# Kernel tuning notes

Hardware: AMD Instinct MI355X
Metric: run time of the kernel (lower is better)

## Reference

```python
import jax, jax.numpy as jnp
import numpy as np

N_NODES = 100000
N_EDGES = 400000
D = 128           # vector_dim
N_GRAPHS = 4096
N_LAYERS = 5
IN_FEAT = 11


def setup_inputs() -> dict:
    key = jax.random.key(0)
    ks = jax.random.split(key, 6)
    x = jax.random.uniform(ks[0], (N_NODES, IN_FEAT), dtype=jnp.float32)
    edge_index = jax.random.randint(ks[1], (2, N_EDGES), 0, N_NODES, dtype=jnp.int64)
    batch = jnp.sort(jax.random.randint(ks[2], (N_NODES,), 0, N_GRAPHS, dtype=jnp.int64))
    # expansion Linear(11, D)
    We = jax.random.normal(ks[3], (IN_FEAT, D), dtype=jnp.float32) * (1.0 / np.sqrt(IN_FEAT))
    be = jnp.zeros((D,), dtype=jnp.float32)
    # stacked GCNConv weights/biases for 5 layers
    Wg = jax.random.normal(ks[4], (N_LAYERS, D, D), dtype=jnp.float32) * (1.0 / np.sqrt(D))
    bg = jnp.zeros((N_LAYERS, D), dtype=jnp.float32)
    return {"x": x, "edge_index": edge_index, "batch": batch, "num_graphs": N_GRAPHS,
            "We": We, "be": be, "Wg": Wg, "bg": bg}


def reference(x, edge_index, batch, num_graphs, We, be, Wg, bg):
    n = x.shape[0]
    src, dst = edge_index[0], edge_index[1]
    # GCNConv(improved=True): self-loop weight 2 -> deg[i] = in_degree + 2
    deg = jax.ops.segment_sum(jnp.ones((src.shape[0],), x.dtype), dst, num_segments=n) + 2.0
    dinv = deg ** -0.5
    enorm = dinv[src] * dinv[dst]          # per-edge symmetric norm [E]
    self_norm = 2.0 * dinv * dinv          # self-loop contribution [N]

    h = jnp.log(x + 1.0) @ We + be         # expansion [N, D]
    for l in range(Wg.shape[0]):
        t = h @ Wg[l]                      # [N, D]
        agg = jax.ops.segment_sum(t[src] * enorm[:, None], dst, num_segments=n)
        agg = agg + self_norm[:, None] * t + bg[l]
        h = h + jax.nn.relu(agg)           # residual; dropout = identity (eval)
    return jax.ops.segment_sum(h, batch, num_segments=num_graphs)  # global_add_pool [G, D]
```

## Files before the change

### kernel.cpp

```cpp
#include <hip/hip_runtime.h>
#include <hip/hip_bf16.h>

#define NN 100000
#define NE 400000
#define DD 128
#define NG 4096
#define NL 5
#define NF 11
#define GROWS 100096

typedef __attribute__((ext_vector_type(8))) __bf16 bf16x8;
typedef __attribute__((ext_vector_type(4))) float f32x4;


__global__ void deg_kernel(const int* __restrict__ ei, int* __restrict__ deg) {
    int e = blockIdx.x * 256 + threadIdx.x;
    if (e < NE) atomicAdd(&deg[ei[NE + e]], 1);
}

__global__ void scan1_kernel(const int* __restrict__ deg, int* __restrict__ off,
                             int* __restrict__ bsums) {
    __shared__ int lds[256];
    int tid = threadIdx.x, b = blockIdx.x;
    int base = b * 1024 + tid * 4;
    int v[4];
#pragma unroll
    for (int q = 0; q < 4; ++q) {
        int i = base + q;
        v[q] = (i < NN) ? deg[i] : 0;
    }
    int s = v[0] + v[1] + v[2] + v[3];
    lds[tid] = s;
    __syncthreads();
    for (int o = 1; o < 256; o <<= 1) {
        int t2 = (tid >= o) ? lds[tid - o] : 0;
        __syncthreads();
        lds[tid] += t2;
        __syncthreads();
    }
    int p = lds[tid] - s;
#pragma unroll
    for (int q = 0; q < 4; ++q) {
        int i = base + q;
        if (i < NN) off[i] = p;
        p += v[q];
    }
    if (tid == 255) bsums[b] = lds[255];
}

__global__ void scan2_kernel(int* __restrict__ bsums, int nb) {
    __shared__ int lds[128];
    int tid = threadIdx.x;
    int v = (tid < nb) ? bsums[tid] : 0;
    lds[tid] = v;
    __syncthreads();
    for (int o = 1; o < 128; o <<= 1) {
        int t2 = (tid >= o) ? lds[tid - o] : 0;
        __syncthreads();
        lds[tid] += t2;
        __syncthreads();
    }
    if (tid < nb) bsums[tid] = lds[tid] - v;
}

__global__ void finish_kernel(int* __restrict__ off, const int* __restrict__ bsums,
                              const int* __restrict__ deg, float* __restrict__ dinv) {
    int i = blockIdx.x * 256 + threadIdx.x;
    if (i == 0) off[NN] = NE;
    if (i < NN) {
        off[i] += bsums[i >> 10];
        dinv[i] = rsqrtf((float)deg[i] + 2.0f);
    }
}

__global__ void fill_kernel(const int* __restrict__ ei, const int* __restrict__ off,
                            int* __restrict__ cursor, int2* __restrict__ csr,
                            const float* __restrict__ dinv) {
    int e = blockIdx.x * 256 + threadIdx.x;
    if (e >= NE) return;
    int s = ei[e];
    int d = ei[NE + e];
    int pos = off[d] + atomicAdd(&cursor[d], 1);
    csr[pos] = make_int2(s, __float_as_int(dinv[s] * dinv[d]));
}


__global__ void wpack_kernel(const float* __restrict__ Wg, unsigned short* __restrict__ whi,
                             unsigned short* __restrict__ wlo) {
    int t = blockIdx.x * 256 + threadIdx.x;
    int l = t >> 14, r = t & 16383;
    int k = r >> 7, n = r & 127;
    float w = Wg[(size_t)l * 16384 + k * 128 + n];
    __bf16 hb = (__bf16)w;
    float lo = w - (float)hb;
    __bf16 lb = (__bf16)lo;
    int ft = n >> 4, kc = k >> 5, lane = (((k >> 3) & 3) << 4) | (n & 15), i = k & 7;
    size_t idx = (size_t)l * 16384 + (((ft * 4 + kc) * 64 + lane) * 8 + i);
    whi[idx] = __builtin_bit_cast(unsigned short, hb);
    wlo[idx] = __builtin_bit_cast(unsigned short, lb);
}


__global__ __launch_bounds__(256) void expand_kernel(const float* __restrict__ x,
                                                     const float* __restrict__ We,
                                                     const float* __restrict__ be,
                                                     float* __restrict__ h) {
    __shared__ float ls[2 * NF];
    const int tid = threadIdx.x;
    const int node0 = blockIdx.x * 2;
    if (tid < 2 * NF) ls[tid] = __logf(x[(size_t)node0 * NF + tid] + 1.0f);
    __syncthreads();
    const int row = tid >> 7, j = tid & 127;
    float acc = be[j];
#pragma unroll
    for (int f = 0; f < NF; ++f) {
        acc = fmaf(ls[row * NF + f], We[f * DD + j], acc);
    }
    h[(size_t)(node0 + row) * DD + j] = acc;
}


__global__ __launch_bounds__(256) void agg_kernel(const float* __restrict__ h,
                                                  unsigned short* __restrict__ gbh,
                                                  unsigned short* __restrict__ gbl,
                                                  const int* __restrict__ off,
                                                  const int2* __restrict__ csr,
                                                  const float* __restrict__ dinv) {
    const int tid = threadIdx.x;
    const int node = blockIdx.x * 8 + (tid >> 5);
    const int jj = tid & 31;
    const float4* __restrict__ h4 = (const float4*)h;

    float di = dinv[node];
    float sn = 2.0f * di * di;
    float4 hv = h4[(size_t)node * 32 + jj];
    float4 acc = make_float4(sn * hv.x, sn * hv.y, sn * hv.z, sn * hv.w);

    const int e0 = off[node];
    const int e1 = off[node + 1];
#pragma unroll 1
    for (int e = e0; e < e1; e += 4) {
        const int eL = e1 - 1;
        int2 r0 = csr[e];
        int2 r1 = csr[min(e + 1, eL)];
        int2 r2 = csr[min(e + 2, eL)];
        int2 r3 = csr[min(e + 3, eL)];
        float4 v0 = h4[(size_t)r0.x * 32 + jj];
        float4 v1 = h4[(size_t)r1.x * 32 + jj];
        float4 v2 = h4[(size_t)r2.x * 32 + jj];
        float4 v3 = h4[(size_t)r3.x * 32 + jj];
        float w0 = __int_as_float(r0.y);
        float w1 = (e + 1 < e1) ? __int_as_float(r1.y) : 0.f;
        float w2 = (e + 2 < e1) ? __int_as_float(r2.y) : 0.f;
        float w3 = (e + 3 < e1) ? __int_as_float(r3.y) : 0.f;
        acc.x = fmaf(w0, v0.x, acc.x); acc.y = fmaf(w0, v0.y, acc.y);
        acc.z = fmaf(w0, v0.z, acc.z); acc.w = fmaf(w0, v0.w, acc.w);
        acc.x = fmaf(w1, v1.x, acc.x); acc.y = fmaf(w1, v1.y, acc.y);
        acc.z = fmaf(w1, v1.z, acc.z); acc.w = fmaf(w1, v1.w, acc.w);
        acc.x = fmaf(w2, v2.x, acc.x); acc.y = fmaf(w2, v2.y, acc.y);
        acc.z = fmaf(w2, v2.z, acc.z); acc.w = fmaf(w2, v2.w, acc.w);
        acc.x = fmaf(w3, v3.x, acc.x); acc.y = fmaf(w3, v3.y, acc.y);
        acc.z = fmaf(w3, v3.z, acc.z); acc.w = fmaf(w3, v3.w, acc.w);
    }

    __bf16 h0 = (__bf16)acc.x; __bf16 l0 = (__bf16)(acc.x - (float)h0);
    __bf16 h1 = (__bf16)acc.y; __bf16 l1 = (__bf16)(acc.y - (float)h1);
    __bf16 h2 = (__bf16)acc.z; __bf16 l2 = (__bf16)(acc.z - (float)h2);
    __bf16 h3 = (__bf16)acc.w; __bf16 l3 = (__bf16)(acc.w - (float)h3);
    const int tile = node >> 4;
    const int kc = jj >> 3;
    const int kg = (jj >> 1) & 3;
    const int i0 = (jj & 1) * 4;
    const int lanep = (kg << 4) | (node & 15);
    size_t base = (((size_t)tile * 4 + kc) * 64 + lanep) * 8 + i0;
    ushort4 hs = make_ushort4(__builtin_bit_cast(unsigned short, h0),
                              __builtin_bit_cast(unsigned short, h1),
                              __builtin_bit_cast(unsigned short, h2),
                              __builtin_bit_cast(unsigned short, h3));
    ushort4 ls = make_ushort4(__builtin_bit_cast(unsigned short, l0),
                              __builtin_bit_cast(unsigned short, l1),
                              __builtin_bit_cast(unsigned short, l2),
                              __builtin_bit_cast(unsigned short, l3));
    *(ushort4*)(gbh + base) = hs;
    *(ushort4*)(gbl + base) = ls;
}


__global__ __launch_bounds__(256) void mfma_gemm(const unsigned short* __restrict__ gbh,
                                                 const unsigned short* __restrict__ gbl,
                                                 float* __restrict__ h,
                                                 const unsigned short* __restrict__ whi,
                                                 const unsigned short* __restrict__ wlo,
                                                 const float* __restrict__ b) {
    const int lane = threadIdx.x & 63;
    const int wv = threadIdx.x >> 6;
    const int nbase = blockIdx.x * 64 + wv * 16;
    const size_t tbase = ((size_t)(nbase >> 4) * 4 * 64 + lane) * 8;

    bf16x8 gh[4], gl[4];
#pragma unroll
    for (int kc = 0; kc < 4; ++kc) {
        gh[kc] = *(const bf16x8*)(gbh + tbase + kc * 512);
        gl[kc] = *(const bf16x8*)(gbl + tbase + kc * 512);
    }

    f32x4 c[8];
#pragma unroll
    for (int ft = 0; ft < 8; ++ft) c[ft] = (f32x4){0.f, 0.f, 0.f, 0.f};

#pragma unroll
    for (int kc = 0; kc < 4; ++kc) {
#pragma unroll
        for (int ft = 0; ft < 8; ++ft) {
            size_t boff = (size_t)(((ft * 4 + kc) * 64 + lane) * 8);
            bf16x8 wh = *(const bf16x8*)(whi + boff);
            bf16x8 wl = *(const bf16x8*)(wlo + boff);
            c[ft] = __builtin_amdgcn_mfma_f32_16x16x32_bf16(wh, gh[kc], c[ft], 0, 0, 0);
            c[ft] = __builtin_amdgcn_mfma_f32_16x16x32_bf16(wl, gh[kc], c[ft], 0, 0, 0);
            c[ft] = __builtin_amdgcn_mfma_f32_16x16x32_bf16(wh, gl[kc], c[ft], 0, 0, 0);
        }
    }

    const int node = nbase + (lane & 15);
    const int f0 = (lane >> 4) * 4;
    if (node < NN) {
#pragma unroll
        for (int ft = 0; ft < 8; ++ft) {
            size_t o = (size_t)node * DD + ft * 16 + f0;
            float4 hv = *(const float4*)(h + o);
            float4 bv = *(const float4*)(b + ft * 16 + f0);
            hv.x += fmaxf(c[ft][0] + bv.x, 0.f);
            hv.y += fmaxf(c[ft][1] + bv.y, 0.f);
            hv.z += fmaxf(c[ft][2] + bv.z, 0.f);
            hv.w += fmaxf(c[ft][3] + bv.w, 0.f);
            *(float4*)(h + o) = hv;
        }
    }
}


__global__ void pool_kernel(const float* __restrict__ h, const int* __restrict__ batch,
                            float* __restrict__ out) {
    int j = threadIdx.x;
    int n0 = blockIdx.x * 64;
    float acc = 0.f;
    int prev = -1;
    for (int n = 0; n < 64; ++n) {
        int i = n0 + n;
        if (i >= NN) break;
        int bi = batch[i];
        if (bi != prev) {
            if (prev >= 0) atomicAdd(&out[(size_t)prev * DD + j], acc);
            acc = 0.f;
            prev = bi;
        }
        acc += h[(size_t)i * DD + j];
    }
    if (prev >= 0) atomicAdd(&out[(size_t)prev * DD + j], acc);
}


static inline size_t align_up(size_t x, size_t a) { return (x + a - 1) & ~(a - 1); }

extern "C" void kernel_launch(void* const* d_in, const int* in_sizes, int n_in,
                              void* d_out, int out_size, void* d_ws, size_t ws_size,
                              hipStream_t stream) {
    const float* x   = (const float*)d_in[0];
    const int*   ei  = (const int*)d_in[1];
    const int*   bat = (const int*)d_in[2];
    const float* We  = (const float*)d_in[4];
    const float* be  = (const float*)d_in[5];
    const float* Wg  = (const float*)d_in[6];
    const float* bg  = (const float*)d_in[7];
    float* out = (float*)d_out;

    char* p = (char*)d_ws;
    size_t o = 0;
    float* h = (float*)(p + o);       o = align_up(o + (size_t)NN * DD * 4, 512);
    unsigned short* gbh = (unsigned short*)(p + o); o = align_up(o + (size_t)GROWS * DD * 2, 512);
    unsigned short* gbl = (unsigned short*)(p + o); o = align_up(o + (size_t)GROWS * DD * 2, 512);
    float* dinv = (float*)(p + o);    o = align_up(o + (size_t)NN * 4, 512);
    int* deg = (int*)(p + o);         o = align_up(o + (size_t)NN * 4, 512);
    int* cursor = (int*)(p + o);      o = align_up(o + (size_t)NN * 4, 512);
    int* off = (int*)(p + o);         o = align_up(o + (size_t)(NN + 1) * 4, 512);
    int* bsums = (int*)(p + o);       o = align_up(o + 512, 512);
    int2* csr = (int2*)(p + o);       o = align_up(o + (size_t)NE * 8, 512);
    unsigned short* whi = (unsigned short*)(p + o); o = align_up(o + (size_t)NL * 16384 * 2, 512);
    unsigned short* wlo = (unsigned short*)(p + o); o = align_up(o + (size_t)NL * 16384 * 2, 512);
    (void)ws_size; (void)in_sizes; (void)n_in; (void)out_size;

    const int GRID_E = (NE + 255) / 256;
    const int GRID_SCAN1 = (NN + 1023) / 1024;
    const int GRID_N256 = (NN + 255) / 256;
    const int GRID_EXP = NN / 2;
    const int GRID_AGG = NN / 8;
    const int GRID_GEMM = GROWS / 64;
    const int GRID_POOL = (NN + 63) / 64;
    const int GRID_WPACK = NL * 16384 / 256;

    hipMemsetAsync(deg, 0, (size_t)NN * 4, stream);
    hipMemsetAsync(cursor, 0, (size_t)NN * 4, stream);
    hipMemsetAsync(out, 0, (size_t)NG * DD * 4, stream);

    deg_kernel<<<GRID_E, 256, 0, stream>>>(ei, deg);
    scan1_kernel<<<GRID_SCAN1, 256, 0, stream>>>(deg, off, bsums);
    scan2_kernel<<<1, 128, 0, stream>>>(bsums, GRID_SCAN1);
    finish_kernel<<<GRID_N256, 256, 0, stream>>>(off, bsums, deg, dinv);
    fill_kernel<<<GRID_E, 256, 0, stream>>>(ei, off, cursor, csr, dinv);
    wpack_kernel<<<GRID_WPACK, 256, 0, stream>>>(Wg, whi, wlo);

    expand_kernel<<<GRID_EXP, 256, 0, stream>>>(x, We, be, h);

    for (int l = 0; l < NL; ++l) {
        agg_kernel<<<GRID_AGG, 256, 0, stream>>>(h, gbh, gbl, off, csr, dinv);
        mfma_gemm<<<GRID_GEMM, 256, 0, stream>>>(gbh, gbl, h,
                                                 whi + (size_t)l * 16384,
                                                 wlo + (size_t)l * 16384,
                                                 bg + (size_t)l * DD);
    }

    pool_kernel<<<GRID_POOL, 128, 0, stream>>>(h, bat, out);
}
```

Baseline: 601.9 us.

## Drop cursor array via in-place offset atomics, batch expand and widen GEMM tiles

The CSR fill now atomically bumps the exclusive offsets in place, so afterwards off[d] holds the end of segment d. The aggregation reads the segment as off[node-1]..off[node], which removes the cursor buffer and its memset. The expansion kernel handles 8 nodes per block and keeps the We column in registers to reuse it. The MFMA GEMM handles 32 nodes per wave instead of 16, reusing each loaded weight fragment across two node tiles at the cost of more registers.

```diff
diff --git a/kernel.cpp b/kernel.cpp
--- a/kernel.cpp
+++ b/kernel.cpp
@@ -66,21 +66,19 @@
 __global__ void finish_kernel(int* __restrict__ off, const int* __restrict__ bsums,
                               const int* __restrict__ deg, float* __restrict__ dinv) {
     int i = blockIdx.x * 256 + threadIdx.x;
-    if (i == 0) off[NN] = NE;
     if (i < NN) {
         off[i] += bsums[i >> 10];
         dinv[i] = rsqrtf((float)deg[i] + 2.0f);
     }
 }
 
-__global__ void fill_kernel(const int* __restrict__ ei, const int* __restrict__ off,
-                            int* __restrict__ cursor, int2* __restrict__ csr,
-                            const float* __restrict__ dinv) {
+__global__ void fill_kernel(const int* __restrict__ ei, int* __restrict__ off,
+                            int2* __restrict__ csr, const float* __restrict__ dinv) {
     int e = blockIdx.x * 256 + threadIdx.x;
     if (e >= NE) return;
     int s = ei[e];
     int d = ei[NE + e];
-    int pos = off[d] + atomicAdd(&cursor[d], 1);
+    int pos = atomicAdd(&off[d], 1);
     csr[pos] = make_int2(s, __float_as_int(dinv[s] * dinv[d]));
 }
 
@@ -105,18 +103,23 @@
                                                      const float* __restrict__ We,
                                                      const float* __restrict__ be,
                                                      float* __restrict__ h) {
-    __shared__ float ls[2 * NF];
+    __shared__ float ls[8 * NF];
     const int tid = threadIdx.x;
-    const int node0 = blockIdx.x * 2;
-    if (tid < 2 * NF) ls[tid] = __logf(x[(size_t)node0 * NF + tid] + 1.0f);
+    const int node0 = blockIdx.x * 8;
+    if (tid < 8 * NF) ls[tid] = __logf(x[(size_t)node0 * NF + tid] + 1.0f);
     __syncthreads();
-    const int row = tid >> 7, j = tid & 127;
-    float acc = be[j];
-#pragma unroll
-    for (int f = 0; f < NF; ++f) {
-        acc = fmaf(ls[row * NF + f], We[f * DD + j], acc);
-    }
-    h[(size_t)(node0 + row) * DD + j] = acc;
+    const int j = tid & 127;
+    float wv[NF], acc0 = be[j];
+#pragma unroll
+    for (int f = 0; f < NF; ++f) wv[f] = We[f * DD + j];
+#pragma unroll
+    for (int r = 0; r < 4; ++r) {
+        const int nl = r * 2 + (tid >> 7);
+        float acc = acc0;
+#pragma unroll
+        for (int f = 0; f < NF; ++f) acc = fmaf(ls[nl * NF + f], wv[f], acc);
+        h[(size_t)(node0 + nl) * DD + j] = acc;
+    }
 }
 
 
@@ -136,8 +139,8 @@
     float4 hv = h4[(size_t)node * 32 + jj];
     float4 acc = make_float4(sn * hv.x, sn * hv.y, sn * hv.z, sn * hv.w);
 
-    const int e0 = off[node];
-    const int e1 = off[node + 1];
+    const int e0 = (node == 0) ? 0 : off[node - 1];
+    const int e1 = off[node];
 #pragma unroll 1
     for (int e = e0; e < e1; e += 4) {
         const int eL = e1 - 1;
@@ -173,16 +176,14 @@
     const int i0 = (jj & 1) * 4;
     const int lanep = (kg << 4) | (node & 15);
     size_t base = (((size_t)tile * 4 + kc) * 64 + lanep) * 8 + i0;
-    ushort4 hs = make_ushort4(__builtin_bit_cast(unsigned short, h0),
-                              __builtin_bit_cast(unsigned short, h1),
-                              __builtin_bit_cast(unsigned short, h2),
-                              __builtin_bit_cast(unsigned short, h3));
-    ushort4 ls = make_ushort4(__builtin_bit_cast(unsigned short, l0),
-                              __builtin_bit_cast(unsigned short, l1),
-                              __builtin_bit_cast(unsigned short, l2),
-                              __builtin_bit_cast(unsigned short, l3));
-    *(ushort4*)(gbh + base) = hs;
-    *(ushort4*)(gbl + base) = ls;
+    *(ushort4*)(gbh + base) = make_ushort4(__builtin_bit_cast(unsigned short, h0),
+                                           __builtin_bit_cast(unsigned short, h1),
+                                           __builtin_bit_cast(unsigned short, h2),
+                                           __builtin_bit_cast(unsigned short, h3));
+    *(ushort4*)(gbl + base) = make_ushort4(__builtin_bit_cast(unsigned short, l0),
+                                           __builtin_bit_cast(unsigned short, l1),
+                                           __builtin_bit_cast(unsigned short, l2),
+                                           __builtin_bit_cast(unsigned short, l3));
 }
 
 
@@ -194,19 +195,23 @@
                                                  const float* __restrict__ b) {
     const int lane = threadIdx.x & 63;
     const int wv = threadIdx.x >> 6;
-    const int nbase = blockIdx.x * 64 + wv * 16;
+    const int nbase = blockIdx.x * 128 + wv * 32;
     const size_t tbase = ((size_t)(nbase >> 4) * 4 * 64 + lane) * 8;
 
-    bf16x8 gh[4], gl[4];
-#pragma unroll
-    for (int kc = 0; kc < 4; ++kc) {
-        gh[kc] = *(const bf16x8*)(gbh + tbase + kc * 512);
-        gl[kc] = *(const bf16x8*)(gbl + tbase + kc * 512);
-    }
-
-    f32x4 c[8];
-#pragma unroll
-    for (int ft = 0; ft < 8; ++ft) c[ft] = (f32x4){0.f, 0.f, 0.f, 0.f};
+    bf16x8 gh[2][4], gl[2][4];
+#pragma unroll
+    for (int nt = 0; nt < 2; ++nt)
+#pragma unroll
+        for (int kc = 0; kc < 4; ++kc) {
+            gh[nt][kc] = *(const bf16x8*)(gbh + tbase + nt * 2048 + kc * 512);
+            gl[nt][kc] = *(const bf16x8*)(gbl + tbase + nt * 2048 + kc * 512);
+        }
+
+    f32x4 c[2][8];
+#pragma unroll
+    for (int nt = 0; nt < 2; ++nt)
+#pragma unroll
+        for (int ft = 0; ft < 8; ++ft) c[nt][ft] = (f32x4){0.f, 0.f, 0.f, 0.f};
 
 #pragma unroll
     for (int kc = 0; kc < 4; ++kc) {
@@ -215,25 +220,31 @@
             size_t boff = (size_t)(((ft * 4 + kc) * 64 + lane) * 8);
             bf16x8 wh = *(const bf16x8*)(whi + boff);
             bf16x8 wl = *(const bf16x8*)(wlo + boff);
-            c[ft] = __builtin_amdgcn_mfma_f32_16x16x32_bf16(wh, gh[kc], c[ft], 0, 0, 0);
-            c[ft] = __builtin_amdgcn_mfma_f32_16x16x32_bf16(wl, gh[kc], c[ft], 0, 0, 0);
-            c[ft] = __builtin_amdgcn_mfma_f32_16x16x32_bf16(wh, gl[kc], c[ft], 0, 0, 0);
+#pragma unroll
+            for (int nt = 0; nt < 2; ++nt) {
+                c[nt][ft] = __builtin_amdgcn_mfma_f32_16x16x32_bf16(wh, gh[nt][kc], c[nt][ft], 0, 0, 0);
+                c[nt][ft] = __builtin_amdgcn_mfma_f32_16x16x32_bf16(wl, gh[nt][kc], c[nt][ft], 0, 0, 0);
+                c[nt][ft] = __builtin_amdgcn_mfma_f32_16x16x32_bf16(wh, gl[nt][kc], c[nt][ft], 0, 0, 0);
+            }
         }
     }
 
-    const int node = nbase + (lane & 15);
     const int f0 = (lane >> 4) * 4;
-    if (node < NN) {
-#pragma unroll
-        for (int ft = 0; ft < 8; ++ft) {
-            size_t o = (size_t)node * DD + ft * 16 + f0;
-            float4 hv = *(const float4*)(h + o);
-            float4 bv = *(const float4*)(b + ft * 16 + f0);
-            hv.x += fmaxf(c[ft][0] + bv.x, 0.f);
-            hv.y += fmaxf(c[ft][1] + bv.y, 0.f);
-            hv.z += fmaxf(c[ft][2] + bv.z, 0.f);
-            hv.w += fmaxf(c[ft][3] + bv.w, 0.f);
-            *(float4*)(h + o) = hv;
+#pragma unroll
+    for (int nt = 0; nt < 2; ++nt) {
+        const int node = nbase + nt * 16 + (lane & 15);
+        if (node < NN) {
+#pragma unroll
+            for (int ft = 0; ft < 8; ++ft) {
+                size_t o = (size_t)node * DD + ft * 16 + f0;
+                float4 hv = *(const float4*)(h + o);
+                float4 bv = *(const float4*)(b + ft * 16 + f0);
+                hv.x += fmaxf(c[nt][ft][0] + bv.x, 0.f);
+                hv.y += fmaxf(c[nt][ft][1] + bv.y, 0.f);
+                hv.z += fmaxf(c[nt][ft][2] + bv.z, 0.f);
+                hv.w += fmaxf(c[nt][ft][3] + bv.w, 0.f);
+                *(float4*)(h + o) = hv;
+            }
         }
     }
 }
@@ -281,7 +292,6 @@
     unsigned short* gbl = (unsigned short*)(p + o); o = align_up(o + (size_t)GROWS * DD * 2, 512);
     float* dinv = (float*)(p + o);    o = align_up(o + (size_t)NN * 4, 512);
     int* deg = (int*)(p + o);         o = align_up(o + (size_t)NN * 4, 512);
-    int* cursor = (int*)(p + o);      o = align_up(o + (size_t)NN * 4, 512);
     int* off = (int*)(p + o);         o = align_up(o + (size_t)(NN + 1) * 4, 512);
     int* bsums = (int*)(p + o);       o = align_up(o + 512, 512);
     int2* csr = (int2*)(p + o);       o = align_up(o + (size_t)NE * 8, 512);
@@ -292,21 +302,20 @@
     const int GRID_E = (NE + 255) / 256;
     const int GRID_SCAN1 = (NN + 1023) / 1024;
     const int GRID_N256 = (NN + 255) / 256;
-    const int GRID_EXP = NN / 2;
+    const int GRID_EXP = NN / 8;
     const int GRID_AGG = NN / 8;
-    const int GRID_GEMM = GROWS / 64;
+    const int GRID_GEMM = GROWS / 128;
     const int GRID_POOL = (NN + 63) / 64;
     const int GRID_WPACK = NL * 16384 / 256;
 
     hipMemsetAsync(deg, 0, (size_t)NN * 4, stream);
-    hipMemsetAsync(cursor, 0, (size_t)NN * 4, stream);
     hipMemsetAsync(out, 0, (size_t)NG * DD * 4, stream);
 
     deg_kernel<<<GRID_E, 256, 0, stream>>>(ei, deg);
     scan1_kernel<<<GRID_SCAN1, 256, 0, stream>>>(deg, off, bsums);
     scan2_kernel<<<1, 128, 0, stream>>>(bsums, GRID_SCAN1);
     finish_kernel<<<GRID_N256, 256, 0, stream>>>(off, bsums, deg, dinv);
-    fill_kernel<<<GRID_E, 256, 0, stream>>>(ei, off, cursor, csr, dinv);
+    fill_kernel<<<GRID_E, 256, 0, stream>>>(ei, off, csr, dinv);
     wpack_kernel<<<GRID_WPACK, 256, 0, stream>>>(Wg, whi, wlo);
 
     expand_kernel<<<GRID_EXP, 256, 0, stream>>>(x, We, be, h);
```

Result: faster. 581.8 us (-3.3%).
